# Optimization experiments

Measured on AMD Instinct MI355X. Metric: run time of the kernel, lower is better.

The kernel has to match this reference:

```python
import jax, jax.numpy as jnp
import numpy as np

THRESHOLD = 0.1  # interaction_threshold

def setup_inputs() -> dict:
    key = jax.random.key(0)
    ks = jax.random.split(key, 12)
    B, F, K, H = 262144, 256, 20, 64
    M = H // 2
    inp = {
        "x": jax.random.normal(ks[0], (B, F), dtype=jnp.float32),
        "interaction_weights": jax.random.normal(ks[1], (F, F), dtype=jnp.float32) * 0.1,
        # context selector: Linear(F,H) -> ReLU -> Linear(H,K) -> Sigmoid
        "Wc1": jax.random.normal(ks[2], (F, H), dtype=jnp.float32) * (1.0 / np.sqrt(F)),
        "bc1": jnp.zeros((H,), dtype=jnp.float32),
        "Wc2": jax.random.normal(ks[3], (H, K), dtype=jnp.float32) * (1.0 / np.sqrt(H)),
        "bc2": jnp.zeros((K,), dtype=jnp.float32),
        # K stacked pair-MLPs: (2->H) ReLU (H->M) ReLU (M->1), dropout inactive (eval)
        "W1": jax.random.normal(ks[4], (K, 2, H), dtype=jnp.float32) * (1.0 / np.sqrt(2.0)),
        "b1": jnp.zeros((K, H), dtype=jnp.float32),
        "W2": jax.random.normal(ks[5], (K, H, M), dtype=jnp.float32) * (1.0 / np.sqrt(H)),
        "b2": jnp.zeros((K, M), dtype=jnp.float32),
        "W3": jax.random.normal(ks[6], (K, M), dtype=jnp.float32) * (1.0 / np.sqrt(M)),
        "b3": jnp.zeros((K,), dtype=jnp.float32),
    }
    return inp


def reference(x, interaction_weights, Wc1, bc1, Wc2, bc2, W1, b1, W2, b2, W3, b3):
    F = interaction_weights.shape[0]
    K = W1.shape[0]
    # strict upper-triangular pair selection (row-major, matching torch.nonzero order)
    ti, tj = jnp.triu_indices(F, k=1)
    scores = jax.nn.sigmoid(interaction_weights)          # triu mask applied by selection
    flat_scores = scores[ti, tj]
    top_vals, top_idx = jax.lax.top_k(flat_scores, K)     # sorted descending like torch.topk
    pi, pj = ti[top_idx], tj[top_idx]                     # [K], [K]
    # gather feature pairs: [B, K, 2]
    pair = jnp.stack([x[:, pi], x[:, pj]], axis=-1)
    # batched tiny MLPs across K interactions (dropout = identity in eval)
    h1 = jax.nn.relu(jnp.einsum('bkp,kph->bkh', pair, W1) + b1)   # [B,K,H]
    h2 = jax.nn.relu(jnp.einsum('bkh,khm->bkm', h1, W2) + b2)     # [B,K,M]
    out = jnp.einsum('bkm,km->bk', h2, W3) + b3                   # [B,K]
    # context weights
    ctx = jax.nn.sigmoid(jax.nn.relu(x @ Wc1 + bc1) @ Wc2 + bc2)  # [B,K]
    interaction_features = out * ctx                              # [B,K]
    importances = top_vals                                        # [K]
    context_weights_mean = ctx.mean(axis=0)                       # [K]
    active_interactions = jnp.sum(top_vals > THRESHOLD)
    selected_pairs = jnp.stack([pi, pj], axis=1)                  # [K,2]
    return (interaction_features, importances, context_weights_mean,
            active_interactions, selected_pairs)
```

## Files before the change

kernel.cpp:

```cpp
#include <hip/hip_runtime.h>
#include <math.h>

#define BTOT 262144
#define FDIM 256
#define KK 20
#define HH 64
#define MM 32

#define IMP_OFF  (BTOT * KK)
#define CWM_OFF  (IMP_OFF + KK)
#define ACT_OFF  (CWM_OFF + KK)
#define PAIR_OFF (ACT_OFF + 1)

__device__ __forceinline__ bool better(float v2, int p2, float v1, int p1) {
  return (v2 > v1) || (v2 == v1 && p2 < p1);
}

__global__ void topk_stage1(const float* __restrict__ w,
                            float* __restrict__ cand_v, int* __restrict__ cand_p) {
  const int i = blockIdx.x;
  const int j = threadIdx.x;
  const int lane = j & 63, wid = j >> 6;
  __shared__ float sv[256];
  __shared__ float rv[4];
  __shared__ int rp[4];

  sv[j] = (j > i) ? w[i * 256 + j] : -1e30f;
  __syncthreads();

  for (int r = 0; r < 20; ++r) {
    float v = sv[j];
    int p = i * 256 + j;
    #pragma unroll
    for (int off = 32; off; off >>= 1) {
      float v2 = __shfl_down(v, off);
      int p2 = __shfl_down(p, off);
      if (better(v2, p2, v, p)) { v = v2; p = p2; }
    }
    if (lane == 0) { rv[wid] = v; rp[wid] = p; }
    __syncthreads();
    if (j == 0) {
      #pragma unroll
      for (int t = 1; t < 4; ++t)
        if (better(rv[t], rp[t], v, p)) { v = rv[t]; p = rp[t]; }
      cand_v[i * 20 + r] = v;
      cand_p[i * 20 + r] = p;
      sv[p & 255] = -2e30f;
    }
    __syncthreads();
  }
}

#define NC 5120
__global__ void topk_stage2(const float* __restrict__ cand_v, const int* __restrict__ cand_p,
                            int* __restrict__ pij, float* __restrict__ out) {
  const int tid = threadIdx.x;
  const int lane = tid & 63, wid = tid >> 6;
  __shared__ float sv[NC];
  __shared__ int sp[NC];
  __shared__ float rv[4];
  __shared__ int rp[4], rq[4];
  __shared__ float selv[20];
  __shared__ int selp[20];

  for (int t = tid; t < NC; t += 256) { sv[t] = cand_v[t]; sp[t] = cand_p[t]; }
  __syncthreads();

  for (int r = 0; r < 20; ++r) {
    float v = -4e30f;
    int p = 0x7fffffff, q = 0;
    for (int t = tid; t < NC; t += 256) {
      float vv = sv[t];
      int pp = sp[t];
      if (better(vv, pp, v, p)) { v = vv; p = pp; q = t; }
    }
    #pragma unroll
    for (int off = 32; off; off >>= 1) {
      float v2 = __shfl_down(v, off);
      int p2 = __shfl_down(p, off);
      int q2 = __shfl_down(q, off);
      if (better(v2, p2, v, p)) { v = v2; p = p2; q = q2; }
    }
    if (lane == 0) { rv[wid] = v; rp[wid] = p; rq[wid] = q; }
    __syncthreads();
    if (tid == 0) {
      #pragma unroll
      for (int t = 1; t < 4; ++t)
        if (better(rv[t], rp[t], v, p)) { v = rv[t]; p = rp[t]; q = rq[t]; }
      selv[r] = v;
      selp[r] = p;
      sv[q] = -3e30f;
    }
    __syncthreads();
  }

  if (tid == 0) {
    int active = 0;
    for (int r = 0; r < 20; ++r) {
      int p = selp[r];
      int i = p >> 8, j = p & 255;
      float s = 1.0f / (1.0f + expf(-selv[r]));
      out[IMP_OFF + r] = s;
      out[PAIR_OFF + 2 * r] = (float)i;
      out[PAIR_OFF + 2 * r + 1] = (float)j;
      if (s > 0.1f) active++;
      pij[r] = i;
      pij[20 + r] = j;
    }
    out[ACT_OFF] = (float)active;
  }
}

#define FCH 32
#define NCHUNK (FDIM / FCH)
#define XSTR 33

__global__ __launch_bounds__(256, 3) void id_main(
    const float* __restrict__ x,
    const float* __restrict__ Wc1, const float* __restrict__ bc1,
    const float* __restrict__ Wc2, const float* __restrict__ bc2,
    const float* __restrict__ W1, const float* __restrict__ b1,
    const float* __restrict__ W2, const float* __restrict__ b2,
    const float* __restrict__ W3, const float* __restrict__ b3,
    const int* __restrict__ pij,
    float* __restrict__ ctx_sums,
    float* __restrict__ out) {
  __shared__ __align__(16) float xs[256 * XSTR];
  __shared__ float csum[KK];

  const int tid = threadIdx.x;
  const int b0 = blockIdx.x * 256;
  if (tid < KK) csum[tid] = 0.0f;

  int pcol[2 * KK];
  #pragma unroll
  for (int i = 0; i < 2 * KK; ++i) pcol[i] = pij[i];

  float h[HH];
  #pragma unroll
  for (int j = 0; j < HH; ++j) h[j] = bc1[j];
  float pv[2 * KK];
  #pragma unroll
  for (int i = 0; i < 2 * KK; ++i) pv[i] = 0.0f;

  const int srow = tid >> 3;
  const int quad = tid & 7;
  const float* __restrict__ xrow_lds = &xs[tid * XSTR];

  #pragma unroll 1
  for (int c = 0; c < NCHUNK; ++c) {
    const int f0 = c * FCH;
    __syncthreads();
    const float* __restrict__ xg = x + (size_t)(b0 + srow) * FDIM + f0 + quad * 4;
    #pragma unroll
    for (int r = 0; r < 8; ++r) {
      const float4 v = *(const float4*)(xg + (size_t)r * 32 * FDIM);
      float* d = &xs[(srow + r * 32) * XSTR + quad * 4];
      d[0] = v.x; d[1] = v.y; d[2] = v.z; d[3] = v.w;
    }
    __syncthreads();
    #pragma unroll 2
    for (int f = 0; f < FCH; ++f) {
      const float xv = xrow_lds[f];
      const float* __restrict__ w0 = Wc1 + (size_t)(f0 + f) * HH;
      #pragma unroll
      for (int j = 0; j < HH; ++j) h[j] = fmaf(xv, w0[j], h[j]);
    }
    #pragma unroll
    for (int i = 0; i < 2 * KK; ++i) {
      const int cc = pcol[i];
      if (cc >= f0 && cc < f0 + FCH) pv[i] = xrow_lds[cc - f0];
    }
  }

  float ctx[KK];
  #pragma unroll
  for (int k = 0; k < KK; ++k) ctx[k] = bc2[k];
  #pragma unroll 2
  for (int j = 0; j < HH; ++j) {
    const float hj = fmaxf(h[j], 0.0f);
    const float* __restrict__ wr = Wc2 + j * KK;
    #pragma unroll
    for (int k = 0; k < KK; ++k) ctx[k] = fmaf(hj, wr[k], ctx[k]);
  }
  #pragma unroll
  for (int k = 0; k < KK; ++k) ctx[k] = 1.0f / (1.0f + expf(-ctx[k]));

  __syncthreads();
  float* __restrict__ so = xs;

  #pragma unroll 1
  for (int k = 0; k < KK; ++k) {
    const float pa = pv[k];
    const float pb = pv[KK + k];
    const float* __restrict__ w1k = W1 + (size_t)k * 2 * HH;
    const float* __restrict__ b1k = b1 + (size_t)k * HH;
    const float* __restrict__ w2k = W2 + (size_t)k * HH * MM;
    const float* __restrict__ b2k = b2 + (size_t)k * MM;

    float h2[MM];
    #pragma unroll
    for (int m = 0; m < MM; ++m) h2[m] = b2k[m];

    #pragma unroll 1
    for (int half = 0; half < 2; ++half) {
      float h1[32];
      #pragma unroll
      for (int j = 0; j < 32; ++j) {
        const int jj = half * 32 + j;
        h1[j] = fmaxf(fmaf(pa, w1k[jj], fmaf(pb, w1k[HH + jj], b1k[jj])), 0.0f);
      }
      const float* __restrict__ w2h = w2k + half * 32 * MM;
      #pragma unroll 2
      for (int j = 0; j < 32; ++j) {
        const float hj = h1[j];
        const float* __restrict__ wr = w2h + j * MM;
        #pragma unroll
        for (int m = 0; m < MM; ++m) h2[m] = fmaf(hj, wr[m], h2[m]);
      }
    }

    const float* __restrict__ w3k = W3 + (size_t)k * MM;
    float o = b3[k];
    #pragma unroll
    for (int m = 0; m < MM; ++m) o = fmaf(fmaxf(h2[m], 0.0f), w3k[m], o);

    so[tid * KK + k] = o * ctx[k];
  }

  const int lane = tid & 63;
  #pragma unroll 1
  for (int k = 0; k < KK; ++k) {
    float v = ctx[k];
    #pragma unroll
    for (int off = 32; off; off >>= 1) v += __shfl_down(v, off);
    if (lane == 0) atomicAdd(&csum[k], v);
  }
  __syncthreads();
  if (tid < KK) atomicAdd(&ctx_sums[tid], csum[tid]);

  const float4* __restrict__ sof = (const float4*)so;
  float4* __restrict__ og = (float4*)(out + (size_t)b0 * KK);
  #pragma unroll
  for (int i = 0; i < 5; ++i) og[tid + i * 256] = sof[tid + i * 256];
}

__global__ void id_finalize(const float* __restrict__ ctx_sums, float* __restrict__ out) {
  const int k = threadIdx.x;
  if (k < KK) out[CWM_OFF + k] = ctx_sums[k] * (1.0f / (float)BTOT);
}

extern "C" void kernel_launch(void* const* d_in, const int* in_sizes, int n_in,
                              void* d_out, int out_size, void* d_ws, size_t ws_size,
                              hipStream_t stream) {
  const float* x   = (const float*)d_in[0];
  const float* iw  = (const float*)d_in[1];
  const float* Wc1 = (const float*)d_in[2];
  const float* bc1 = (const float*)d_in[3];
  const float* Wc2 = (const float*)d_in[4];
  const float* bc2 = (const float*)d_in[5];
  const float* W1  = (const float*)d_in[6];
  const float* b1  = (const float*)d_in[7];
  const float* W2  = (const float*)d_in[8];
  const float* b2  = (const float*)d_in[9];
  const float* W3  = (const float*)d_in[10];
  const float* b3  = (const float*)d_in[11];
  float* out = (float*)d_out;

  float* wsf    = (float*)d_ws;
  float* cand_v = wsf;
  int*   cand_p = (int*)(wsf + 5120);
  int*   pij    = (int*)(wsf + 10240);
  float* csums  = wsf + 10280;

  hipMemsetAsync(csums, 0, KK * sizeof(float), stream);
  topk_stage1<<<256, 256, 0, stream>>>(iw, cand_v, cand_p);
  topk_stage2<<<1, 256, 0, stream>>>(cand_v, cand_p, pij, out);
  id_main<<<BTOT / 256, 256, 0, stream>>>(x, Wc1, bc1, Wc2, bc2, W1, b1, W2, b2, W3, b3,
                                          pij, csums, out);
  id_finalize<<<1, 64, 0, stream>>>(csums, out);
}
```

Measured before the change: 1.110 ms.

## Move pair values to LDS, fully unroll MLP loops, pad output staging

Gathered pair feature values now go to a shared-memory array instead of a 40-entry register array. The hidden-layer loops are fully unrolled over all 64 units rather than processed in two halves. The context-sum reduction is moved before the MLP loop. The output staging buffer uses a padded stride of 21 to avoid LDS bank conflicts, and the ctx multiply is applied afterwards. Launch bounds drop from 3 to 2 blocks per CU, trading occupancy for more registers and larger unrolled bodies, while the extra 40KB of LDS per block also limits occupancy.

Result: slower. 1.732 ms (+56.1%).

```diff
diff --git a/kernel.cpp b/kernel.cpp
--- a/kernel.cpp
+++ b/kernel.cpp
@@ -111,11 +111,10 @@
   }
 }
 
-#define FCH 32
-#define NCHUNK (FDIM / FCH)
 #define XSTR 33
-
-__global__ __launch_bounds__(256, 3) void id_main(
+#define SOSTR 21
+
+__global__ __launch_bounds__(256, 2) void id_main(
     const float* __restrict__ x,
     const float* __restrict__ Wc1, const float* __restrict__ bc1,
     const float* __restrict__ Wc2, const float* __restrict__ bc2,
@@ -126,6 +125,7 @@
     float* __restrict__ ctx_sums,
     float* __restrict__ out) {
   __shared__ __align__(16) float xs[256 * XSTR];
+  __shared__ float pvs[2 * KK * 256];
   __shared__ float csum[KK];
 
   const int tid = threadIdx.x;
@@ -139,17 +139,13 @@
   float h[HH];
   #pragma unroll
   for (int j = 0; j < HH; ++j) h[j] = bc1[j];
-  float pv[2 * KK];
-  #pragma unroll
-  for (int i = 0; i < 2 * KK; ++i) pv[i] = 0.0f;
 
   const int srow = tid >> 3;
   const int quad = tid & 7;
-  const float* __restrict__ xrow_lds = &xs[tid * XSTR];
 
   #pragma unroll 1
-  for (int c = 0; c < NCHUNK; ++c) {
-    const int f0 = c * FCH;
+  for (int c = 0; c < 8; ++c) {
+    const int f0 = c * 32;
     __syncthreads();
     const float* __restrict__ xg = x + (size_t)(b0 + srow) * FDIM + f0 + quad * 4;
     #pragma unroll
@@ -159,9 +155,10 @@
       d[0] = v.x; d[1] = v.y; d[2] = v.z; d[3] = v.w;
     }
     __syncthreads();
-    #pragma unroll 2
-    for (int f = 0; f < FCH; ++f) {
-      const float xv = xrow_lds[f];
+    const float* __restrict__ xrow = &xs[tid * XSTR];
+    #pragma unroll 1
+    for (int f = 0; f < 32; ++f) {
+      const float xv = xrow[f];
       const float* __restrict__ w0 = Wc1 + (size_t)(f0 + f) * HH;
       #pragma unroll
       for (int j = 0; j < HH; ++j) h[j] = fmaf(xv, w0[j], h[j]);
@@ -169,80 +166,84 @@
     #pragma unroll
     for (int i = 0; i < 2 * KK; ++i) {
       const int cc = pcol[i];
-      if (cc >= f0 && cc < f0 + FCH) pv[i] = xrow_lds[cc - f0];
+      if (cc >= f0 && cc < f0 + 32) pvs[i * 256 + tid] = xrow[cc - f0];
     }
   }
 
   float ctx[KK];
   #pragma unroll
   for (int k = 0; k < KK; ++k) ctx[k] = bc2[k];
-  #pragma unroll 2
+  #pragma unroll
   for (int j = 0; j < HH; ++j) {
     const float hj = fmaxf(h[j], 0.0f);
-    const float* __restrict__ wr = Wc2 + j * KK;
-    #pragma unroll
-    for (int k = 0; k < KK; ++k) ctx[k] = fmaf(hj, wr[k], ctx[k]);
+    #pragma unroll
+    for (int k = 0; k < KK; ++k) ctx[k] = fmaf(hj, Wc2[j * KK + k], ctx[k]);
   }
   #pragma unroll
   for (int k = 0; k < KK; ++k) ctx[k] = 1.0f / (1.0f + expf(-ctx[k]));
+
+  const int lane = tid & 63;
+  #pragma unroll
+  for (int k = 0; k < KK; ++k) {
+    float v = ctx[k];
+    #pragma unroll
+    for (int off = 32; off; off >>= 1) v += __shfl_down(v, off);
+    if (lane == 0) atomicAdd(&csum[k], v);
+  }
 
   __syncthreads();
   float* __restrict__ so = xs;
 
   #pragma unroll 1
   for (int k = 0; k < KK; ++k) {
-    const float pa = pv[k];
-    const float pb = pv[KK + k];
+    const float pa = pvs[k * 256 + tid];
+    const float pb = pvs[(KK + k) * 256 + tid];
     const float* __restrict__ w1k = W1 + (size_t)k * 2 * HH;
     const float* __restrict__ b1k = b1 + (size_t)k * HH;
     const float* __restrict__ w2k = W2 + (size_t)k * HH * MM;
     const float* __restrict__ b2k = b2 + (size_t)k * MM;
+    const float* __restrict__ w3k = W3 + (size_t)k * MM;
+
+    float h1[HH];
+    #pragma unroll
+    for (int j = 0; j < HH; ++j)
+      h1[j] = fmaxf(fmaf(pa, w1k[j], fmaf(pb, w1k[HH + j], b1k[j])), 0.0f);
 
     float h2[MM];
     #pragma unroll
     for (int m = 0; m < MM; ++m) h2[m] = b2k[m];
-
-    #pragma unroll 1
-    for (int half = 0; half < 2; ++half) {
-      float h1[32];
-      #pragma unroll
-      for (int j = 0; j < 32; ++j) {
-        const int jj = half * 32 + j;
-        h1[j] = fmaxf(fmaf(pa, w1k[jj], fmaf(pb, w1k[HH + jj], b1k[jj])), 0.0f);
-      }
-      const float* __restrict__ w2h = w2k + half * 32 * MM;
-      #pragma unroll 2
-      for (int j = 0; j < 32; ++j) {
-        const float hj = h1[j];
-        const float* __restrict__ wr = w2h + j * MM;
-        #pragma unroll
-        for (int m = 0; m < MM; ++m) h2[m] = fmaf(hj, wr[m], h2[m]);
-      }
-    }
-
-    const float* __restrict__ w3k = W3 + (size_t)k * MM;
+    #pragma unroll
+    for (int j = 0; j < HH; ++j) {
+      const float hj = h1[j];
+      const float* __restrict__ wr = w2k + j * MM;
+      #pragma unroll
+      for (int m = 0; m < MM; ++m) h2[m] = fmaf(hj, wr[m], h2[m]);
+    }
+
     float o = b3[k];
     #pragma unroll
     for (int m = 0; m < MM; ++m) o = fmaf(fmaxf(h2[m], 0.0f), w3k[m], o);
 
-    so[tid * KK + k] = o * ctx[k];
-  }
-
-  const int lane = tid & 63;
-  #pragma unroll 1
-  for (int k = 0; k < KK; ++k) {
-    float v = ctx[k];
-    #pragma unroll
-    for (int off = 32; off; off >>= 1) v += __shfl_down(v, off);
-    if (lane == 0) atomicAdd(&csum[k], v);
-  }
+    so[tid * SOSTR + k] = o;
+  }
+
+  #pragma unroll
+  for (int k = 0; k < KK; ++k) so[tid * SOSTR + k] *= ctx[k];
+
   __syncthreads();
   if (tid < KK) atomicAdd(&ctx_sums[tid], csum[tid]);
 
-  const float4* __restrict__ sof = (const float4*)so;
-  float4* __restrict__ og = (float4*)(out + (size_t)b0 * KK);
-  #pragma unroll
-  for (int i = 0; i < 5; ++i) og[tid + i * 256] = sof[tid + i * 256];
+  float* __restrict__ og = out + (size_t)b0 * KK;
+  #pragma unroll
+  for (int i = 0; i < 5; ++i) {
+    const int e = (tid + i * 256) * 4;
+    float4 v;
+    v.x = so[((e    ) / KK) * SOSTR + (e    ) % KK];
+    v.y = so[((e + 1) / KK) * SOSTR + (e + 1) % KK];
+    v.z = so[((e + 2) / KK) * SOSTR + (e + 2) % KK];
+    v.w = so[((e + 3) / KK) * SOSTR + (e + 3) % KK];
+    *(float4*)(og + e) = v;
+  }
 }
 
 __global__ void id_finalize(const float* __restrict__ ctx_sums, float* __restrict__ out) {
```
